# Optimization experiments

Measured on AMD Instinct MI355X. Metric: run time of the kernel, lower is better.

The kernel has to match this reference:

```python
import jax, jax.numpy as jnp
import numpy as np

N_NODES = 50000
N_EDGES = 800000
D = 64          # encoder output dim (encoder.out)
MLP_DIM = 64    # mlp_edge_model hidden dim


def setup_inputs() -> dict:
    key = jax.random.key(0)
    ks = jax.random.split(key, 8)
    x = jax.random.normal(ks[0], (N_NODES, D), dtype=jnp.float32)
    edge_index = jax.random.randint(ks[1], (2, N_EDGES), 0, N_NODES, dtype=jnp.int64)
    # xavier-ish scaled weights
    W_enc = jax.random.normal(ks[2], (D, D), dtype=jnp.float32) * (1.0 / np.sqrt(D))
    b_enc = jnp.zeros((D,), dtype=jnp.float32)
    W1 = jax.random.normal(ks[3], (2 * D, MLP_DIM), dtype=jnp.float32) * (1.0 / np.sqrt(2 * D))
    b1 = jnp.zeros((MLP_DIM,), dtype=jnp.float32)
    W2 = jax.random.normal(ks[4], (MLP_DIM, 1), dtype=jnp.float32) * (1.0 / np.sqrt(MLP_DIM))
    b2 = jnp.zeros((1,), dtype=jnp.float32)
    return {"x": x, "edge_index": edge_index, "W_enc": W_enc, "b_enc": b_enc,
            "W1": W1, "b1": b1, "W2": W2, "b2": b2}


def reference(x, edge_index, W_enc, b_enc, W1, b1, W2, b2):
    src, dst = edge_index[0], edge_index[1]
    # --- encoder: 1-layer message-passing GCN stand-in ---
    agg = jax.ops.segment_sum(x[src], dst, num_segments=N_NODES)   # [N, D]
    node_emb = jax.nn.relu((x + agg) @ W_enc + b_enc)              # [N, D]
    # --- gather src/dst embeddings, concat, 2-layer MLP edge scorer ---
    edge_emb = jnp.concatenate([node_emb[src], node_emb[dst]], axis=1)  # [E, 2D]
    h = jax.nn.relu(edge_emb @ W1 + b1)                            # [E, mlp_dim]
    edge_logits = h @ W2 + b2                                      # [E, 1]
    return edge_logits
```

## Files before the change

kernel.cpp:

```cpp
#include <hip/hip_runtime.h>
#include <hip/hip_bf16.h>
#include <stdint.h>

#define N_NODES 50000
#define N_EDGES 800000
#define D 64
#define VROWS 50048
#define CVT_BLOCKS 3125
#define CAP 64

typedef __hip_bfloat16 bf16;
typedef __bf16 bf16x8 __attribute__((ext_vector_type(8)));
typedef float  f32x4  __attribute__((ext_vector_type(4)));

__device__ __forceinline__ float bu2f(unsigned short u) {
    unsigned int w = ((unsigned int)u) << 16;
    return __builtin_bit_cast(float, w);
}
__device__ __forceinline__ unsigned short f2bu(float f) {
    bf16 h = __float2bfloat16(f);
    return __builtin_bit_cast(unsigned short, h);
}
__device__ __forceinline__ float ldf(const void* p, size_t i, bool f32mode) {
    if (f32mode) return ((const float*)p)[i];
    return bu2f(((const unsigned short*)p)[i]);
}
__device__ __forceinline__ void stf(void* p, size_t i, float v, bool f32mode) {
    if (f32mode) ((float*)p)[i] = v;
    else ((unsigned short*)p)[i] = f2bu(v);
}
__device__ __forceinline__ int ldidx(const int* ei, size_t e, int row, bool i64mode) {
    if (i64mode) return ei[((size_t)row * N_EDGES + e) * 2];
    return ei[(size_t)row * N_EDGES + e];
}
__device__ __forceinline__ void unpack8(uint4 v, float* f) {
    f[0] = bu2f(v.x & 0xffff); f[1] = bu2f(v.x >> 16);
    f[2] = bu2f(v.y & 0xffff); f[3] = bu2f(v.y >> 16);
    f[4] = bu2f(v.z & 0xffff); f[5] = bu2f(v.z >> 16);
    f[6] = bu2f(v.w & 0xffff); f[7] = bu2f(v.w >> 16);
}

__global__ __launch_bounds__(256) void init_kernel(
    const void* __restrict__ x, const int* __restrict__ ei,
    const void* __restrict__ W2, const void* __restrict__ b1,
    const void* __restrict__ b2,
    int* __restrict__ flags, unsigned short* __restrict__ w2bf,
    float* __restrict__ b1f, float* __restrict__ b2fp,
    int* __restrict__ counts,
    unsigned short* __restrict__ xbf,
    unsigned short* __restrict__ dst16, unsigned short* __restrict__ src16)
{
    __shared__ int sh_f32m, sh_i64m;
    int tid = threadIdx.x;

    if (tid < 64) {
        const unsigned short* u = (const unsigned short*)x;
        int weird = 0, zeros = 0;
        #pragma unroll
        for (int k = tid; k < 128; k += 64) {
            int ex = (u[2 * k] >> 7) & 0xFF;
            if (ex < 90 || ex > 160) ++weird;
            if (ei[2 * k + 1] == 0) ++zeros;
        }
        #pragma unroll
        for (int off = 1; off < 64; off <<= 1) {
            weird += __shfl_xor(weird, off, 64);
            zeros += __shfl_xor(zeros, off, 64);
        }
        if (tid == 0) {
            sh_f32m = (weird > 32) ? 1 : 0;
            sh_i64m = (zeros > 120) ? 1 : 0;
        }
    }
    __syncthreads();
    bool f32m = sh_f32m != 0;
    bool i64m = sh_i64m != 0;

    if (blockIdx.x == 0) {
        if (tid < 64) {
            w2bf[tid] = f2bu(ldf(W2, tid, f32m));
            b1f[tid]  = ldf(b1, tid, f32m);
        }
        if (tid == 0) {
            flags[0] = f32m ? 1 : 0;
            flags[1] = sh_i64m;
            b2fp[0] = ldf(b2, 0, f32m);
        }
    }

    int cbase = blockIdx.x * 16 + (tid & 15);
    if (tid < 16 && cbase < N_NODES) counts[cbase] = 0;

    int e = blockIdx.x * 256 + tid;
    dst16[e] = (unsigned short)ldidx(ei, e, 1, i64m);
    src16[e] = (unsigned short)ldidx(ei, e, 0, i64m);

    size_t idx4 = (size_t)blockIdx.x * 256 + tid;
    if (f32m) {
        float4 fv = ((const float4*)x)[idx4];
        ushort4 o;
        o.x = f2bu(fv.x); o.y = f2bu(fv.y); o.z = f2bu(fv.z); o.w = f2bu(fv.w);
        ((ushort4*)xbf)[idx4] = o;
    } else {
        ((uint2*)xbf)[idx4] = ((const uint2*)x)[idx4];
    }
}

__global__ __launch_bounds__(256) void histfill_kernel(
    const unsigned short* __restrict__ dst16,
    const unsigned short* __restrict__ src16,
    int* __restrict__ counts, uint2* __restrict__ epack)
{
    int region = blockIdx.x >> 3;
    int grp    = blockIdx.x & 7;
    int e0 = region * 2048 + threadIdx.x * 8;
    if (e0 >= N_EDGES) return;
    uint4 dv = *(const uint4*)(dst16 + e0);
    uint4 sv = *(const uint4*)(src16 + e0);
    unsigned int dw[4] = {dv.x, dv.y, dv.z, dv.w};
    unsigned int sw[4] = {sv.x, sv.y, sv.z, sv.w};
    #pragma unroll
    for (int k = 0; k < 8; ++k) {
        if (e0 + k >= N_EDGES) break;
        int d = (int)((dw[k >> 1] >> ((k & 1) * 16)) & 0xffffu);
        if (((d >> 6) & 7) != grp) continue;
        int s = (int)((sw[k >> 1] >> ((k & 1) * 16)) & 0xffffu);
        int r = atomicAdd(&counts[d], 1);
        if (r < CAP) {
            uint2 v;
            v.x = (unsigned int)s;
            v.y = (unsigned int)(e0 + k);
            epack[(size_t)d * CAP + r] = v;
        }
    }
}

__global__ __launch_bounds__(256) void gather_kernel(
    const unsigned short* __restrict__ xbf,
    const int* __restrict__ counts, const uint2* __restrict__ epack,
    unsigned short* __restrict__ vtab)
{
    int w    = (blockIdx.x * 256 + threadIdx.x) >> 6;
    int lane = threadIdx.x & 63;
    if (w >= N_NODES) return;
    int cnt = counts[w];
    if (cnt > CAP) cnt = CAP;
    int beg = w * CAP, end = beg + cnt;
    int f8   = lane & 7;
    int slot = lane >> 3;

    float acc[8] = {0.f, 0.f, 0.f, 0.f, 0.f, 0.f, 0.f, 0.f};
    if (slot == 0) {
        uint4 q = ((const uint4*)xbf)[(size_t)w * 8 + f8];
        unpack8(q, acc);
    }

    int j = beg;
    for (; j + 16 <= end; j += 16) {
        int s0 = (int)epack[j + slot].x;
        int s1 = (int)epack[j + 8 + slot].x;
        uint4 q0 = ((const uint4*)xbf)[(size_t)s0 * 8 + f8];
        uint4 q1 = ((const uint4*)xbf)[(size_t)s1 * 8 + f8];
        float f0[8], f1[8];
        unpack8(q0, f0);
        unpack8(q1, f1);
        #pragma unroll
        for (int i = 0; i < 8; ++i) acc[i] += f0[i] + f1[i];
    }
    for (; j < end; j += 8) {
        int e = j + slot;
        bool ok = e < end;
        int s = (int)epack[ok ? e : beg].x;
        uint4 q = ((const uint4*)xbf)[(size_t)s * 8 + f8];
        float f[8];
        unpack8(q, f);
        if (ok) {
            #pragma unroll
            for (int i = 0; i < 8; ++i) acc[i] += f[i];
        }
    }

    #pragma unroll
    for (int i = 0; i < 8; ++i) {
        acc[i] += __shfl_xor(acc[i], 8, 64);
        acc[i] += __shfl_xor(acc[i], 16, 64);
        acc[i] += __shfl_xor(acc[i], 32, 64);
    }

    if (slot == 0) {
        uint4 o;
        o.x = (unsigned int)f2bu(acc[0]) | ((unsigned int)f2bu(acc[1]) << 16);
        o.y = (unsigned int)f2bu(acc[2]) | ((unsigned int)f2bu(acc[3]) << 16);
        o.z = (unsigned int)f2bu(acc[4]) | ((unsigned int)f2bu(acc[5]) << 16);
        o.w = (unsigned int)f2bu(acc[6]) | ((unsigned int)f2bu(acc[7]) << 16);
        ((uint4*)vtab)[(size_t)w * 8 + f8] = o;
    }
}

__global__ __launch_bounds__(256) void nodemm_kernel(
    const unsigned short* vtab,
    const void* __restrict__ W_enc, const void* __restrict__ b_enc,
    const void* __restrict__ W1,
    unsigned short* p_src, unsigned short* p_dst,
    const float* __restrict__ b1f, const int* __restrict__ flags)
{
    __shared__ unsigned short wtWe[64 * 72];
    __shared__ unsigned short wtWa[64 * 72];
    __shared__ unsigned short wtWb[64 * 72];
    __shared__ float benc[64];
    __shared__ unsigned short ebuf[4][16 * 72];

    bool f32m = flags[0] != 0;
    int tid = threadIdx.x;
    for (int t = tid; t < 4096; t += 256) {
        int i = t >> 6, j = t & 63;
        wtWe[j * 72 + i] = f2bu(ldf(W_enc, t, f32m));
        wtWa[j * 72 + i] = f2bu(ldf(W1, t, f32m));
        wtWb[j * 72 + i] = f2bu(ldf(W1, 4096 + t, f32m));
    }
    if (tid < 64) benc[tid] = ldf(b_enc, tid, f32m);
    __syncthreads();

    int wave = tid >> 6;
    int lane = tid & 63;
    int lo   = lane & 15;
    int quad = lane >> 4;
    unsigned short* eb = ebuf[wave];
    int base = blockIdx.x * 64 + wave * 16;

    bf16x8 av0 = *(const bf16x8*)&vtab[(size_t)(base + lo) * D + quad * 8];
    bf16x8 av1 = *(const bf16x8*)&vtab[(size_t)(base + lo) * D + 32 + quad * 8];

    f32x4 z = {0.f, 0.f, 0.f, 0.f};
    f32x4 acc1[4] = {z, z, z, z};
    #pragma unroll
    for (int nt = 0; nt < 4; ++nt) {
        bf16x8 b0  = *(const bf16x8*)&wtWe[(nt * 16 + lo) * 72 + quad * 8];
        bf16x8 b1v = *(const bf16x8*)&wtWe[(nt * 16 + lo) * 72 + 32 + quad * 8];
        acc1[nt] = __builtin_amdgcn_mfma_f32_16x16x32_bf16(av0, b0, acc1[nt], 0, 0, 0);
        acc1[nt] = __builtin_amdgcn_mfma_f32_16x16x32_bf16(av1, b1v, acc1[nt], 0, 0, 0);
    }
    #pragma unroll
    for (int nt = 0; nt < 4; ++nt) {
        float bias = benc[nt * 16 + lo];
        #pragma unroll
        for (int r = 0; r < 4; ++r) {
            int m = quad * 4 + r;
            float ev = fmaxf(acc1[nt][r] + bias, 0.f);
            eb[m * 72 + nt * 16 + lo] = f2bu(ev);
        }
    }

    bf16x8 ae0 = *(const bf16x8*)&eb[lo * 72 + quad * 8];
    bf16x8 ae1 = *(const bf16x8*)&eb[lo * 72 + 32 + quad * 8];

    f32x4 acc2[4] = {z, z, z, z};
    f32x4 acc3[4] = {z, z, z, z};
    #pragma unroll
    for (int nt = 0; nt < 4; ++nt) {
        bf16x8 ba0 = *(const bf16x8*)&wtWa[(nt * 16 + lo) * 72 + quad * 8];
        bf16x8 ba1 = *(const bf16x8*)&wtWa[(nt * 16 + lo) * 72 + 32 + quad * 8];
        bf16x8 bb0 = *(const bf16x8*)&wtWb[(nt * 16 + lo) * 72 + quad * 8];
        bf16x8 bb1 = *(const bf16x8*)&wtWb[(nt * 16 + lo) * 72 + 32 + quad * 8];
        acc2[nt] = __builtin_amdgcn_mfma_f32_16x16x32_bf16(ae0, ba0, acc2[nt], 0, 0, 0);
        acc2[nt] = __builtin_amdgcn_mfma_f32_16x16x32_bf16(ae1, ba1, acc2[nt], 0, 0, 0);
        acc3[nt] = __builtin_amdgcn_mfma_f32_16x16x32_bf16(ae0, bb0, acc3[nt], 0, 0, 0);
        acc3[nt] = __builtin_amdgcn_mfma_f32_16x16x32_bf16(ae1, bb1, acc3[nt], 0, 0, 0);
    }
    #pragma unroll
    for (int nt = 0; nt < 4; ++nt) {
        float b1v = b1f[nt * 16 + lo];
        #pragma unroll
        for (int r = 0; r < 4; ++r) {
            int node = base + quad * 4 + r;
            if (node < N_NODES) {
                size_t idx = (size_t)node * D + nt * 16 + lo;
                p_src[idx] = f2bu(acc2[nt][r] + b1v);
                p_dst[idx] = f2bu(acc3[nt][r]);
            }
        }
    }
}

__global__ __launch_bounds__(256) void edge_kernel(
    const unsigned short* __restrict__ p_src,
    const unsigned short* __restrict__ p_dst,
    const int* __restrict__ counts,
    const uint2* __restrict__ epack,
    const unsigned short* __restrict__ w2bf, const float* __restrict__ b2fp,
    void* __restrict__ out, const int* __restrict__ flags)
{
    bool f32m = flags[0] != 0;
    int w    = (blockIdx.x * 256 + threadIdx.x) >> 6;
    int lane = threadIdx.x & 63;
    if (w >= N_NODES) return;
    int cnt = counts[w];
    if (cnt > CAP) cnt = CAP;
    if (cnt == 0) return;
    int beg = w * CAP, end = beg + cnt;

    int sub = lane & 7;
    int g   = lane >> 3;

    uint4 pdv = ((const uint4*)p_dst)[(size_t)w * 8 + sub];
    uint4 w2v = ((const uint4*)w2bf)[sub];
    float pd[8], w2[8];
    unpack8(pdv, pd);
    unpack8(w2v, w2);
    float bb = b2fp[0];

    int j = beg;
    for (; j + 16 <= end; j += 16) {
        int p0 = j + g, p1 = j + 8 + g;
        uint2 e0 = epack[p0];
        uint2 e1 = epack[p1];
        uint4 q0 = ((const uint4*)p_src)[(size_t)e0.x * 8 + sub];
        uint4 q1 = ((const uint4*)p_src)[(size_t)e1.x * 8 + sub];
        float f0[8], f1[8];
        unpack8(q0, f0);
        unpack8(q1, f1);
        float c0 = 0.f, c1 = 0.f;
        #pragma unroll
        for (int i = 0; i < 8; ++i) {
            c0 += fmaxf(f0[i] + pd[i], 0.f) * w2[i];
            c1 += fmaxf(f1[i] + pd[i], 0.f) * w2[i];
        }
        c0 += __shfl_xor(c0, 1, 64);
        c0 += __shfl_xor(c0, 2, 64);
        c0 += __shfl_xor(c0, 4, 64);
        c1 += __shfl_xor(c1, 1, 64);
        c1 += __shfl_xor(c1, 2, 64);
        c1 += __shfl_xor(c1, 4, 64);
        if (sub == 0) {
            stf(out, e0.y, c0 + bb, f32m);
            stf(out, e1.y, c1 + bb, f32m);
        }
    }
    for (; j < end; j += 8) {
        int pos = j + g;
        bool ok = pos < end;
        uint2 ev = epack[ok ? pos : beg];
        uint4 psv = ((const uint4*)p_src)[(size_t)ev.x * 8 + sub];
        float ps[8];
        unpack8(psv, ps);
        float c = 0.f;
        #pragma unroll
        for (int i = 0; i < 8; ++i)
            c += fmaxf(ps[i] + pd[i], 0.f) * w2[i];
        c += __shfl_xor(c, 1, 64);
        c += __shfl_xor(c, 2, 64);
        c += __shfl_xor(c, 4, 64);
        if (sub == 0 && ok) {
            stf(out, ev.y, c + bb, f32m);
        }
    }
}

extern "C" void kernel_launch(void* const* d_in, const int* in_sizes, int n_in,
                              void* d_out, int out_size, void* d_ws, size_t ws_size,
                              hipStream_t stream)
{
    const void* x     = d_in[0];
    const int*  ei    = (const int*)d_in[1];
    const void* W_enc = d_in[2];
    const void* b_enc = d_in[3];
    const void* W1    = d_in[4];
    const void* b1    = d_in[5];
    const void* W2    = d_in[6];
    const void* b2    = d_in[7];

    const size_t NTv  = (size_t)VROWS * D;
    const size_t NCAP = (size_t)N_NODES * CAP;
    unsigned short* p_src = (unsigned short*)d_ws;
    unsigned short* p_dst = p_src + NTv;
    unsigned short* xbf   = p_dst + NTv;
    uint2* epack   = (uint2*)(xbf + NTv);
    float* b1f     = (float*)(epack + NCAP);
    unsigned short* w2bf = (unsigned short*)(b1f + 64);
    float* b2fp    = (float*)(w2bf + 64);
    int*   counts  = (int*)(b2fp + 4);
    int*   flags   = counts + N_NODES;
    unsigned short* dst16 = (unsigned short*)(flags + 2);
    unsigned short* src16 = dst16 + N_EDGES;

    unsigned short* vtab = p_src;

    init_kernel<<<CVT_BLOCKS, 256, 0, stream>>>(x, ei, W2, b1, b2, flags, w2bf,
                                                b1f, b2fp, counts, xbf,
                                                dst16, src16);

    const int HF_BLOCKS = ((N_EDGES + 2047) / 2048) * 8;
    histfill_kernel<<<HF_BLOCKS, 256, 0, stream>>>(dst16, src16, counts, epack);

    const int NWB = (N_NODES * 64 + 255) / 256;
    gather_kernel<<<NWB, 256, 0, stream>>>(xbf, counts, epack, vtab);
    nodemm_kernel<<<(N_NODES + 63) / 64, 256, 0, stream>>>(vtab, W_enc, b_enc, W1,
                                                           p_src, p_dst, b1f, flags);
    edge_kernel<<<NWB, 256, 0, stream>>>(p_src, p_dst, counts, epack,
                                         w2bf, b2fp, d_out, flags);
}
```

Measured before the change: 191.5 us.

## Score edges in original order and shrink CSR entries to 16-bit source ids

The edge scorer now walks edges in their original order, 16 per wave, reading src16/dst16 directly. Outputs are written contiguously instead of scattered through the bucketed edge list. The bucket array drops the packed edge id and keeps only a 16-bit source index, which cuts histfill writes and gather-kernel reads. In exchange, each edge now gathers its p_dst row at random instead of reusing it per destination node, so that bandwidth must come from cache.

```diff
diff --git a/kernel.cpp b/kernel.cpp
--- a/kernel.cpp
+++ b/kernel.cpp
@@ -109,7 +109,7 @@
 __global__ __launch_bounds__(256) void histfill_kernel(
     const unsigned short* __restrict__ dst16,
     const unsigned short* __restrict__ src16,
-    int* __restrict__ counts, uint2* __restrict__ epack)
+    int* __restrict__ counts, unsigned short* __restrict__ sarr)
 {
     int region = blockIdx.x >> 3;
     int grp    = blockIdx.x & 7;
@@ -124,20 +124,16 @@
         if (e0 + k >= N_EDGES) break;
         int d = (int)((dw[k >> 1] >> ((k & 1) * 16)) & 0xffffu);
         if (((d >> 6) & 7) != grp) continue;
-        int s = (int)((sw[k >> 1] >> ((k & 1) * 16)) & 0xffffu);
         int r = atomicAdd(&counts[d], 1);
-        if (r < CAP) {
-            uint2 v;
-            v.x = (unsigned int)s;
-            v.y = (unsigned int)(e0 + k);
-            epack[(size_t)d * CAP + r] = v;
-        }
+        if (r < CAP)
+            sarr[(size_t)d * CAP + r] =
+                (unsigned short)((sw[k >> 1] >> ((k & 1) * 16)) & 0xffffu);
     }
 }
 
 __global__ __launch_bounds__(256) void gather_kernel(
     const unsigned short* __restrict__ xbf,
-    const int* __restrict__ counts, const uint2* __restrict__ epack,
+    const int* __restrict__ counts, const unsigned short* __restrict__ sarr,
     unsigned short* __restrict__ vtab)
 {
     int w    = (blockIdx.x * 256 + threadIdx.x) >> 6;
@@ -157,8 +153,8 @@
 
     int j = beg;
     for (; j + 16 <= end; j += 16) {
-        int s0 = (int)epack[j + slot].x;
-        int s1 = (int)epack[j + 8 + slot].x;
+        int s0 = sarr[j + slot];
+        int s1 = sarr[j + 8 + slot];
         uint4 q0 = ((const uint4*)xbf)[(size_t)s0 * 8 + f8];
         uint4 q1 = ((const uint4*)xbf)[(size_t)s1 * 8 + f8];
         float f0[8], f1[8];
@@ -170,7 +166,7 @@
     for (; j < end; j += 8) {
         int e = j + slot;
         bool ok = e < end;
-        int s = (int)epack[ok ? e : beg].x;
+        int s = sarr[ok ? e : beg];
         uint4 q = ((const uint4*)xbf)[(size_t)s * 8 + f8];
         float f[8];
         unpack8(q, f);
@@ -285,74 +281,54 @@
 __global__ __launch_bounds__(256) void edge_kernel(
     const unsigned short* __restrict__ p_src,
     const unsigned short* __restrict__ p_dst,
-    const int* __restrict__ counts,
-    const uint2* __restrict__ epack,
+    const unsigned short* __restrict__ src16,
+    const unsigned short* __restrict__ dst16,
     const unsigned short* __restrict__ w2bf, const float* __restrict__ b2fp,
     void* __restrict__ out, const int* __restrict__ flags)
 {
     bool f32m = flags[0] != 0;
-    int w    = (blockIdx.x * 256 + threadIdx.x) >> 6;
+    int wid  = (blockIdx.x * 256 + threadIdx.x) >> 6;
     int lane = threadIdx.x & 63;
-    if (w >= N_NODES) return;
-    int cnt = counts[w];
-    if (cnt > CAP) cnt = CAP;
-    if (cnt == 0) return;
-    int beg = w * CAP, end = beg + cnt;
-
+    int e_base = wid * 16;
+    if (e_base >= N_EDGES) return;
+    int g   = lane >> 3;
     int sub = lane & 7;
-    int g   = lane >> 3;
-
-    uint4 pdv = ((const uint4*)p_dst)[(size_t)w * 8 + sub];
+
     uint4 w2v = ((const uint4*)w2bf)[sub];
-    float pd[8], w2[8];
-    unpack8(pdv, pd);
+    float w2[8];
     unpack8(w2v, w2);
     float bb = b2fp[0];
 
-    int j = beg;
-    for (; j + 16 <= end; j += 16) {
-        int p0 = j + g, p1 = j + 8 + g;
-        uint2 e0 = epack[p0];
-        uint2 e1 = epack[p1];
-        uint4 q0 = ((const uint4*)p_src)[(size_t)e0.x * 8 + sub];
-        uint4 q1 = ((const uint4*)p_src)[(size_t)e1.x * 8 + sub];
-        float f0[8], f1[8];
-        unpack8(q0, f0);
-        unpack8(q1, f1);
-        float c0 = 0.f, c1 = 0.f;
-        #pragma unroll
-        for (int i = 0; i < 8; ++i) {
-            c0 += fmaxf(f0[i] + pd[i], 0.f) * w2[i];
-            c1 += fmaxf(f1[i] + pd[i], 0.f) * w2[i];
-        }
-        c0 += __shfl_xor(c0, 1, 64);
-        c0 += __shfl_xor(c0, 2, 64);
-        c0 += __shfl_xor(c0, 4, 64);
-        c1 += __shfl_xor(c1, 1, 64);
-        c1 += __shfl_xor(c1, 2, 64);
-        c1 += __shfl_xor(c1, 4, 64);
-        if (sub == 0) {
-            stf(out, e0.y, c0 + bb, f32m);
-            stf(out, e1.y, c1 + bb, f32m);
-        }
-    }
-    for (; j < end; j += 8) {
-        int pos = j + g;
-        bool ok = pos < end;
-        uint2 ev = epack[ok ? pos : beg];
-        uint4 psv = ((const uint4*)p_src)[(size_t)ev.x * 8 + sub];
-        float ps[8];
-        unpack8(psv, ps);
-        float c = 0.f;
-        #pragma unroll
-        for (int i = 0; i < 8; ++i)
-            c += fmaxf(ps[i] + pd[i], 0.f) * w2[i];
-        c += __shfl_xor(c, 1, 64);
-        c += __shfl_xor(c, 2, 64);
-        c += __shfl_xor(c, 4, 64);
-        if (sub == 0 && ok) {
-            stf(out, ev.y, c + bb, f32m);
-        }
+    int e0 = e_base + g;
+    int e1 = e_base + 8 + g;
+    int s0 = src16[e0], d0 = dst16[e0];
+    int s1 = src16[e1], d1 = dst16[e1];
+
+    uint4 qs0 = ((const uint4*)p_src)[(size_t)s0 * 8 + sub];
+    uint4 qd0 = ((const uint4*)p_dst)[(size_t)d0 * 8 + sub];
+    uint4 qs1 = ((const uint4*)p_src)[(size_t)s1 * 8 + sub];
+    uint4 qd1 = ((const uint4*)p_dst)[(size_t)d1 * 8 + sub];
+    float fs0[8], fd0[8], fs1[8], fd1[8];
+    unpack8(qs0, fs0);
+    unpack8(qd0, fd0);
+    unpack8(qs1, fs1);
+    unpack8(qd1, fd1);
+
+    float c0 = 0.f, c1 = 0.f;
+    #pragma unroll
+    for (int i = 0; i < 8; ++i) {
+        c0 += fmaxf(fs0[i] + fd0[i], 0.f) * w2[i];
+        c1 += fmaxf(fs1[i] + fd1[i], 0.f) * w2[i];
+    }
+    c0 += __shfl_xor(c0, 1, 64);
+    c0 += __shfl_xor(c0, 2, 64);
+    c0 += __shfl_xor(c0, 4, 64);
+    c1 += __shfl_xor(c1, 1, 64);
+    c1 += __shfl_xor(c1, 2, 64);
+    c1 += __shfl_xor(c1, 4, 64);
+    if (sub == 0) {
+        stf(out, e0, c0 + bb, f32m);
+        stf(out, e1, c1 + bb, f32m);
     }
 }
 
@@ -374,13 +350,13 @@
     unsigned short* p_src = (unsigned short*)d_ws;
     unsigned short* p_dst = p_src + NTv;
     unsigned short* xbf   = p_dst + NTv;
-    uint2* epack   = (uint2*)(xbf + NTv);
-    float* b1f     = (float*)(epack + NCAP);
+    unsigned short* sarr  = xbf + NTv;
+    float* b1f     = (float*)(sarr + NCAP);
     unsigned short* w2bf = (unsigned short*)(b1f + 64);
     float* b2fp    = (float*)(w2bf + 64);
     int*   counts  = (int*)(b2fp + 4);
     int*   flags   = counts + N_NODES;
-    unsigned short* dst16 = (unsigned short*)(flags + 2);
+    unsigned short* dst16 = (unsigned short*)(flags + 8);
     unsigned short* src16 = dst16 + N_EDGES;
 
     unsigned short* vtab = p_src;
@@ -390,12 +366,12 @@
                                                 dst16, src16);
 
     const int HF_BLOCKS = ((N_EDGES + 2047) / 2048) * 8;
-    histfill_kernel<<<HF_BLOCKS, 256, 0, stream>>>(dst16, src16, counts, epack);
+    histfill_kernel<<<HF_BLOCKS, 256, 0, stream>>>(dst16, src16, counts, sarr);
 
     const int NWB = (N_NODES * 64 + 255) / 256;
-    gather_kernel<<<NWB, 256, 0, stream>>>(xbf, counts, epack, vtab);
+    gather_kernel<<<NWB, 256, 0, stream>>>(xbf, counts, sarr, vtab);
     nodemm_kernel<<<(N_NODES + 63) / 64, 256, 0, stream>>>(vtab, W_enc, b_enc, W1,
                                                            p_src, p_dst, b1f, flags);
-    edge_kernel<<<NWB, 256, 0, stream>>>(p_src, p_dst, counts, epack,
+    edge_kernel<<<NWB, 256, 0, stream>>>(p_src, p_dst, src16, dst16,
                                          w2bf, b2fp, d_out, flags);
 }
```

After: 182.3 us. 4.8% less time.
